# Optimization experiments

Measured on AMD Instinct MI355X. Metric: run time of the kernel, lower is better.

Reference implementation:

```python
import jax, jax.numpy as jnp
import numpy as np

REGION_INDEX = [[3,0,1,2,4],[7,8,9,10,11],[5,6],[13,12],[14,15,23,24,32,33],[22,21,31,30,40,39],[16,17,18,19,20],[25,26,27,28,29],[34,35,36,37,38],[41,42],[49,48],[43,44,45,46,47],[50,51,57],[56,55,61],[52,53,54],[58,59,60]]
INPUT_SIZE = 5
HIDDEN = 100
REGIONS = 16


def setup_inputs() -> dict:
    key = jax.random.key(0)
    ks = jax.random.split(key, 5)
    features = jax.random.normal(ks[0], (128, 256, 62, INPUT_SIZE), dtype=jnp.float32)
    s = 1.0 / np.sqrt(HIDDEN)  # PyTorch LSTM init scale
    # dir 0 = forward, dir 1 = reverse
    w_ih = jax.random.uniform(ks[1], (REGIONS, 2, 4 * HIDDEN, INPUT_SIZE), jnp.float32, -s, s)
    w_hh = jax.random.uniform(ks[2], (REGIONS, 2, 4 * HIDDEN, HIDDEN), jnp.float32, -s, s)
    b_ih = jax.random.uniform(ks[3], (REGIONS, 2, 4 * HIDDEN), jnp.float32, -s, s)
    b_hh = jax.random.uniform(ks[4], (REGIONS, 2, 4 * HIDDEN), jnp.float32, -s, s)
    return {"features": features, "w_ih": w_ih, "w_hh": w_hh, "b_ih": b_ih, "b_hh": b_hh}


def _lstm_last(x, Wih, Whh, bih, bhh):
    # x: (N, L, I) -> final hidden state h_{L-1}: (N, H). PyTorch gate order i,f,g,o.
    N = x.shape[0]
    H = Whh.shape[1]
    bias = bih + bhh

    def step(carry, xt):
        h, c = carry
        g = xt @ Wih.T + h @ Whh.T + bias
        i, f, gg, o = jnp.split(g, 4, axis=-1)
        c = jax.nn.sigmoid(f) * c + jax.nn.sigmoid(i) * jnp.tanh(gg)
        h = jax.nn.sigmoid(o) * jnp.tanh(c)
        return (h, c), None

    h0 = jnp.zeros((N, H), x.dtype)
    (h, _), _ = jax.lax.scan(step, (h0, h0), jnp.swapaxes(x, 0, 1))
    return h


def _forward(features, w_ih, w_hh, b_ih, b_hh):
    # flatten (B, T, 62, 5) -> (N, 62, 5)
    x = features.reshape(-1, features.shape[2], features.shape[3])
    outs = []
    for r in range(REGIONS):
        idx = jnp.asarray(REGION_INDEX[r])
        xr = x[:, idx, :]  # (N, L_r, 5)
        # forward-direction hidden at last timestep
        h_f = _lstm_last(xr, w_ih[r, 0], w_hh[r, 0], b_ih[r, 0], b_hh[r, 0])
        # reverse-direction output at last position == one step on x[:, -1] from zero state
        h_b = _lstm_last(xr[:, -1:, :], w_ih[r, 1], w_hh[r, 1], b_ih[r, 1], b_hh[r, 1])
        outs.append(jnp.concatenate([h_f, h_b], axis=-1))  # (N, 2H)
    return jnp.stack(outs, axis=1)  # (N, 16, 2H)


def reference(features, w_ih, w_hh, b_ih, b_hh):
    return _forward(features, w_ih, w_hh, b_ih, b_hh)
```

## Files before the change

### kernel.cpp

```cpp
#include <hip/hip_runtime.h>


typedef _Float16 f16;
typedef _Float16 half8 __attribute__((ext_vector_type(8)));
typedef float floatx4 __attribute__((ext_vector_type(4)));

#define FEAT_STRIDE 310
#define AST 136
#define ASZ (64 * AST)
#define OST 104

__constant__ int c_pos[16][6] = {
 {3,0,1,2,4,0},{7,8,9,10,11,0},{5,6,0,0,0,0},{13,12,0,0,0,0},
 {14,15,23,24,32,33},{22,21,31,30,40,39},{16,17,18,19,20,0},{25,26,27,28,29,0},
 {34,35,36,37,38,0},{41,42,0,0,0,0},{49,48,0,0,0,0},{43,44,45,46,47,0},
 {50,51,57,0,0,0},{56,55,61,0,0,0},{52,53,54,0,0,0},{58,59,60,0,0,0}};
__constant__ int c_len[16] = {5,5,2,2,6,6,5,5,5,2,2,5,3,3,3,3};

__device__ __forceinline__ float sigf(float x) {
  return __builtin_amdgcn_rcpf(1.f + __builtin_amdgcn_exp2f(-1.44269504088896f * x));
}
__device__ __forceinline__ float tanhf_fast(float x) {
  return 1.f - 2.f * __builtin_amdgcn_rcpf(1.f + __builtin_amdgcn_exp2f(2.88539008177793f * x));
}

__global__ __launch_bounds__(256) void prep_kernel(
    const float* __restrict__ w_ih, const float* __restrict__ w_hh,
    const float* __restrict__ b_ih, const float* __restrict__ b_hh,
    f16* __restrict__ wp)
{
  int id = blockIdx.x * 256 + threadIdx.x;
  if (id >= 16 * 400 * 128) return;
  int k = id & 127;
  int rowN = (id >> 7) % 400;
  int r = (id >> 7) / 400;
  int j = rowN >> 2, g = rowN & 3;
  int orig = (r * 2 + 0) * 400 + g * 100 + j;
  float v;
  if (k < 100)       v = w_hh[orig * 100 + k];
  else if (k < 105)  v = w_ih[orig * 5 + (k - 100)];
  else if (k == 105) v = b_ih[orig] + b_hh[orig];
  else               v = 0.f;
  wp[id] = (f16)v;
}

__global__ __launch_bounds__(320, 3) void fwd_kernel(
    const float* __restrict__ feat, const f16* __restrict__ wp,
    float* __restrict__ out)
{
  __shared__ __align__(16) f16 Abuf[2 * ASZ];
  float* smemf = (float*)Abuf;

  const int bx = blockIdx.x;
  const int r  = bx >> 9;
  const int n0 = (bx & 511) << 6;
  const int tid  = threadIdx.x;
  const int wave = tid >> 6;
  const int lane = tid & 63;
  const int quad = lane >> 4;
  const int l15  = lane & 15;
  const int T = c_len[r];

  half8 wf[5][4];
  {
    const f16* wr = wp + (size_t)r * 400 * 128;
    #pragma unroll
    for (int tn = 0; tn < 5; ++tn) {
      int row = 16 * (5 * wave + tn) + l15;
      #pragma unroll
      for (int kf = 0; kf < 4; ++kf)
        wf[tn][kf] = *(const half8*)(wr + row * 128 + 32 * kf + 8 * quad);
    }
  }

  for (int i = tid; i < 2 * 64 * 64; i += 320) {
    int buf = i >> 12;
    int rem = i & 4095;
    int m = rem >> 6, kw = rem & 63;
    ((unsigned int*)Abuf)[buf * (ASZ / 2) + m * (AST / 2) + kw] =
        (kw == 52) ? 0x3C000000u : 0u;
  }

  float xv[6];
  const int xm = tid & 63, xs = tid >> 6;
  {
    const float* fb = feat + (size_t)(n0 + xm) * FEAT_STRIDE + xs;
    #pragma unroll
    for (int tt = 0; tt < 6; ++tt)
      if (tt < T) xv[tt] = fb[c_pos[r][tt] * 5];
  }
  __syncthreads();
  Abuf[xm * AST + 100 + xs] = (f16)xv[0];
  __syncthreads();

  float creg[4][5];
  #pragma unroll
  for (int mt = 0; mt < 4; ++mt)
    #pragma unroll
    for (int tn = 0; tn < 5; ++tn) creg[mt][tn] = 0.f;

  for (int t = 0; t < T; ++t) {
    const f16* Acur = Abuf + (t & 1) * ASZ;
    f16* Anxt = Abuf + ((t + 1) & 1) * ASZ;

    if (t + 1 < T) {
      #pragma unroll
      for (int mt = 0; mt < 4; ++mt) {
        half8 bf[4];
        #pragma unroll
        for (int kf = 0; kf < 4; ++kf)
          bf[kf] = *(const half8*)(Acur + (16 * mt + l15) * AST + 32 * kf + 8 * quad);
        #pragma unroll
        for (int tn = 0; tn < 5; ++tn) {
          floatx4 acc = {0.f, 0.f, 0.f, 0.f};
          #pragma unroll
          for (int kf = 0; kf < 4; ++kf)
            acc = __builtin_amdgcn_mfma_f32_16x16x32_f16(wf[tn][kf], bf[kf], acc, 0, 0, 0);
          float ig = sigf(acc[0]);
          float fg = sigf(acc[1]);
          float gg = tanhf_fast(acc[2]);
          float og = sigf(acc[3]);
          float cn = fg * creg[mt][tn] + ig * gg;
          creg[mt][tn] = cn;
          int j = 4 * (5 * wave + tn) + quad;
          Anxt[(16 * mt + l15) * AST + j] = (f16)(og * tanhf_fast(cn));
        }
      }
      Anxt[xm * AST + 100 + xs] = (f16)xv[t + 1];
      __syncthreads();
    } else {
      float hreg[4][5];
      #pragma unroll
      for (int mt = 0; mt < 4; ++mt) {
        half8 bf[4];
        #pragma unroll
        for (int kf = 0; kf < 4; ++kf)
          bf[kf] = *(const half8*)(Acur + (16 * mt + l15) * AST + 32 * kf + 8 * quad);
        #pragma unroll
        for (int tn = 0; tn < 5; ++tn) {
          floatx4 acc = {0.f, 0.f, 0.f, 0.f};
          #pragma unroll
          for (int kf = 0; kf < 4; ++kf)
            acc = __builtin_amdgcn_mfma_f32_16x16x32_f16(wf[tn][kf], bf[kf], acc, 0, 0, 0);
          float ig = sigf(acc[0]);
          float fg = sigf(acc[1]);
          float gg = tanhf_fast(acc[2]);
          float og = sigf(acc[3]);
          float cn = fg * creg[mt][tn] + ig * gg;
          hreg[mt][tn] = og * tanhf_fast(cn);
        }
      }
      __syncthreads();
      #pragma unroll
      for (int mt = 0; mt < 4; ++mt)
        #pragma unroll
        for (int tn = 0; tn < 5; ++tn) {
          int j = 4 * (5 * wave + tn) + quad;
          smemf[(16 * mt + l15) * OST + j] = hreg[mt][tn];
        }
      __syncthreads();
    }
  }

  #pragma unroll
  for (int it = 0; it < 5; ++it) {
    int idx = tid + it * 320;
    int m = idx / 25, ch = idx - m * 25;
    floatx4 v = *(const floatx4*)(smemf + m * OST + ch * 4);
    *(floatx4*)(out + (size_t)(n0 + m) * 3200 + r * 200 + ch * 4) = v;
  }
}

__global__ __launch_bounds__(256) void bwd_kernel(
    const float* __restrict__ feat, const float* __restrict__ w_ih,
    const float* __restrict__ b_ih, const float* __restrict__ b_hh,
    float* __restrict__ out)
{
  __shared__ float wg[300 * 7];
  __shared__ float xs[128 * 5];
  const int bx = blockIdx.x;
  const int r  = bx >> 8;
  const int n0 = (bx & 255) << 7;
  const int tid = threadIdx.x;
  const int pos = c_pos[r][c_len[r] - 1];

  for (int i = tid; i < 2100; i += 256) {
    int row = i / 7, c = i - row * 7;
    int q = row / 100, jj = row - q * 100;
    int qq = (q == 0) ? 0 : (q + 1);
    int orig = (r * 2 + 1) * 400 + qq * 100 + jj;
    float v = 0.f;
    if (c < 5)       v = w_ih[orig * 5 + c];
    else if (c == 5) v = b_ih[orig] + b_hh[orig];
    wg[i] = v;
  }
  for (int i = tid; i < 640; i += 256) {
    int nl = i / 5, s = i - nl * 5;
    xs[i] = feat[(size_t)(n0 + nl) * FEAT_STRIDE + pos * 5 + s];
  }
  __syncthreads();

  if (tid < 200) {
    const int g  = tid / 100;
    const int jj = tid - g * 100;
    const float* wi = wg + jj * 7;
    const float* wc = wg + (100 + jj) * 7;
    const float* wo = wg + (200 + jj) * 7;
    float i0 = wi[0], i1 = wi[1], i2 = wi[2], i3 = wi[3], i4 = wi[4], ib = wi[5];
    float c0 = wc[0], c1 = wc[1], c2 = wc[2], c3 = wc[3], c4 = wc[4], cb = wc[5];
    float o0 = wo[0], o1 = wo[1], o2 = wo[2], o3 = wo[3], o4 = wo[4], ob = wo[5];
    for (int i = 0; i < 64; ++i) {
      int nl = g * 64 + i;
      const float* xp = xs + nl * 5;
      float x0 = xp[0], x1 = xp[1], x2 = xp[2], x3 = xp[3], x4 = xp[4];
      float gi = ib + i0*x0 + i1*x1 + i2*x2 + i3*x3 + i4*x4;
      float gc = cb + c0*x0 + c1*x1 + c2*x2 + c3*x3 + c4*x4;
      float go = ob + o0*x0 + o1*x1 + o2*x2 + o3*x3 + o4*x4;
      float cc = sigf(gi) * tanhf_fast(gc);
      float hh = sigf(go) * tanhf_fast(cc);
      out[(size_t)(n0 + nl) * 3200 + r * 200 + 100 + jj] = hh;
    }
  }
}

extern "C" void kernel_launch(void* const* d_in, const int* in_sizes, int n_in,
                              void* d_out, int out_size, void* d_ws, size_t ws_size,
                              hipStream_t stream) {
  const float* feat = (const float*)d_in[0];
  const float* w_ih = (const float*)d_in[1];
  const float* w_hh = (const float*)d_in[2];
  const float* b_ih = (const float*)d_in[3];
  const float* b_hh = (const float*)d_in[4];
  float* out = (float*)d_out;
  f16* wp = (f16*)d_ws;

  prep_kernel<<<3200, 256, 0, stream>>>(w_ih, w_hh, b_ih, b_hh, wp);
  fwd_kernel<<<8192, 320, 0, stream>>>(feat, wp, out);
  bwd_kernel<<<4096, 256, 0, stream>>>(feat, w_ih, b_ih, b_hh, out);
}
```

Measured before the change: 1.082 ms.

## Stage LSTM weights in LDS and run barrier-free per-wave recurrences

Each workgroup of 512 threads now copies the whole region weight matrix into LDS. Each wave then runs its own 16-row LSTM recurrence over all 400 gate rows in a private LDS state slice, with no block-wide barriers inside the time loop. The last hidden state is written straight to global memory instead of being staged through shared memory. The trade-off is that weight fragments are reloaded from LDS for every MFMA instead of staying in registers. The roughly 155 KB LDS footprint also limits occupancy to one block per CU.

```diff
diff --git a/kernel.cpp b/kernel.cpp
--- a/kernel.cpp
+++ b/kernel.cpp
@@ -6,9 +6,7 @@
 typedef float floatx4 __attribute__((ext_vector_type(4)));
 
 #define FEAT_STRIDE 310
-#define AST 136
-#define ASZ (64 * AST)
-#define OST 104
+#define WST 136
 
 __constant__ int c_pos[16][6] = {
  {3,0,1,2,4,0},{7,8,9,10,11,0},{5,6,0,0,0,0},{13,12,0,0,0,0},
@@ -44,16 +42,18 @@
   wp[id] = (f16)v;
 }
 
-__global__ __launch_bounds__(320, 3) void fwd_kernel(
+__global__ __launch_bounds__(512, 2) void fwd_kernel(
     const float* __restrict__ feat, const f16* __restrict__ wp,
     float* __restrict__ out)
 {
-  __shared__ __align__(16) f16 Abuf[2 * ASZ];
-  float* smemf = (float*)Abuf;
+  __shared__ __align__(16) unsigned char lds_raw[158976];
+  f16*   Wl = (f16*)lds_raw;
+  f16*   Sl = (f16*)(lds_raw + 108800);
+  float* Xl = (float*)(lds_raw + 143616);
 
   const int bx = blockIdx.x;
-  const int r  = bx >> 9;
-  const int n0 = (bx & 511) << 6;
+  const int r  = bx >> 8;
+  const int n0 = (bx & 255) << 7;
   const int tid  = threadIdx.x;
   const int wave = tid >> 6;
   const int lane = tid & 63;
@@ -61,113 +61,67 @@
   const int l15  = lane & 15;
   const int T = c_len[r];
 
-  half8 wf[5][4];
   {
     const f16* wr = wp + (size_t)r * 400 * 128;
-    #pragma unroll
-    for (int tn = 0; tn < 5; ++tn) {
-      int row = 16 * (5 * wave + tn) + l15;
-      #pragma unroll
-      for (int kf = 0; kf < 4; ++kf)
-        wf[tn][kf] = *(const half8*)(wr + row * 128 + 32 * kf + 8 * quad);
+    for (int idx = tid; idx < 400 * 16; idx += 512) {
+      int row = idx >> 4, c = idx & 15;
+      *(half8*)(Wl + row * WST + 8 * c) = *(const half8*)(wr + row * 128 + 8 * c);
     }
   }
-
-  for (int i = tid; i < 2 * 64 * 64; i += 320) {
-    int buf = i >> 12;
-    int rem = i & 4095;
-    int m = rem >> 6, kw = rem & 63;
-    ((unsigned int*)Abuf)[buf * (ASZ / 2) + m * (AST / 2) + kw] =
-        (kw == 52) ? 0x3C000000u : 0u;
+  for (int idx = tid; idx < T * 640; idx += 512) {
+    int t = idx / 640, rem = idx - t * 640;
+    int m = rem / 5, s = rem - m * 5;
+    Xl[idx] = feat[(size_t)(n0 + m) * FEAT_STRIDE + c_pos[r][t] * 5 + s];
   }
-
-  float xv[6];
-  const int xm = tid & 63, xs = tid >> 6;
   {
-    const float* fb = feat + (size_t)(n0 + xm) * FEAT_STRIDE + xs;
-    #pragma unroll
-    for (int tt = 0; tt < 6; ++tt)
-      if (tt < T) xv[tt] = fb[c_pos[r][tt] * 5];
+    unsigned int* Swd = (unsigned int*)Sl;
+    for (int idx = tid; idx < 8 * 16 * (WST / 2); idx += 512) {
+      int kw = idx % (WST / 2);
+      Swd[idx] = (kw == 52) ? 0x3C000000u : 0u;
+    }
   }
   __syncthreads();
-  Abuf[xm * AST + 100 + xs] = (f16)xv[0];
-  __syncthreads();
 
-  float creg[4][5];
+  f16* Sw = Sl + wave * 16 * WST;
+  const int xm = lane >> 2, xsl = lane & 3;
+
+  float creg[25];
   #pragma unroll
-  for (int mt = 0; mt < 4; ++mt)
-    #pragma unroll
-    for (int tn = 0; tn < 5; ++tn) creg[mt][tn] = 0.f;
+  for (int tn = 0; tn < 25; ++tn) creg[tn] = 0.f;
 
   for (int t = 0; t < T; ++t) {
-    const f16* Acur = Abuf + (t & 1) * ASZ;
-    f16* Anxt = Abuf + ((t + 1) & 1) * ASZ;
+    Sw[xm * WST + 100 + xsl] = (f16)Xl[t * 640 + (wave * 16 + xm) * 5 + xsl];
+    if (lane < 16)
+      Sw[l15 * WST + 104] = (f16)Xl[t * 640 + (wave * 16 + l15) * 5 + 4];
 
-    if (t + 1 < T) {
+    half8 bf[4];
+    #pragma unroll
+    for (int kf = 0; kf < 4; ++kf)
+      bf[kf] = *(const half8*)(Sw + l15 * WST + 32 * kf + 8 * quad);
+
+    const bool last = (t + 1 == T);
+    #pragma unroll
+    for (int tn = 0; tn < 25; ++tn) {
+      floatx4 acc = {0.f, 0.f, 0.f, 0.f};
       #pragma unroll
-      for (int mt = 0; mt < 4; ++mt) {
-        half8 bf[4];
-        #pragma unroll
-        for (int kf = 0; kf < 4; ++kf)
-          bf[kf] = *(const half8*)(Acur + (16 * mt + l15) * AST + 32 * kf + 8 * quad);
-        #pragma unroll
-        for (int tn = 0; tn < 5; ++tn) {
-          floatx4 acc = {0.f, 0.f, 0.f, 0.f};
-          #pragma unroll
-          for (int kf = 0; kf < 4; ++kf)
-            acc = __builtin_amdgcn_mfma_f32_16x16x32_f16(wf[tn][kf], bf[kf], acc, 0, 0, 0);
-          float ig = sigf(acc[0]);
-          float fg = sigf(acc[1]);
-          float gg = tanhf_fast(acc[2]);
-          float og = sigf(acc[3]);
-          float cn = fg * creg[mt][tn] + ig * gg;
-          creg[mt][tn] = cn;
-          int j = 4 * (5 * wave + tn) + quad;
-          Anxt[(16 * mt + l15) * AST + j] = (f16)(og * tanhf_fast(cn));
-        }
+      for (int kf = 0; kf < 4; ++kf) {
+        half8 wfr = *(const half8*)(Wl + (16 * tn + l15) * WST + 32 * kf + 8 * quad);
+        acc = __builtin_amdgcn_mfma_f32_16x16x32_f16(wfr, bf[kf], acc, 0, 0, 0);
       }
-      Anxt[xm * AST + 100 + xs] = (f16)xv[t + 1];
-      __syncthreads();
-    } else {
-      float hreg[4][5];
-      #pragma unroll
-      for (int mt = 0; mt < 4; ++mt) {
-        half8 bf[4];
-        #pragma unroll
-        for (int kf = 0; kf < 4; ++kf)
-          bf[kf] = *(const half8*)(Acur + (16 * mt + l15) * AST + 32 * kf + 8 * quad);
-        #pragma unroll
-        for (int tn = 0; tn < 5; ++tn) {
-          floatx4 acc = {0.f, 0.f, 0.f, 0.f};
-          #pragma unroll
-          for (int kf = 0; kf < 4; ++kf)
-            acc = __builtin_amdgcn_mfma_f32_16x16x32_f16(wf[tn][kf], bf[kf], acc, 0, 0, 0);
-          float ig = sigf(acc[0]);
-          float fg = sigf(acc[1]);
-          float gg = tanhf_fast(acc[2]);
-          float og = sigf(acc[3]);
-          float cn = fg * creg[mt][tn] + ig * gg;
-          hreg[mt][tn] = og * tanhf_fast(cn);
-        }
+      float ig = sigf(acc[0]);
+      float fg = sigf(acc[1]);
+      float gg = tanhf_fast(acc[2]);
+      float og = sigf(acc[3]);
+      float cn = fg * creg[tn] + ig * gg;
+      creg[tn] = cn;
+      float hv = og * tanhf_fast(cn);
+      int j = 4 * tn + quad;
+      if (!last) {
+        Sw[l15 * WST + j] = (f16)hv;
+      } else {
+        out[(size_t)(n0 + wave * 16 + l15) * 3200 + r * 200 + j] = hv;
       }
-      __syncthreads();
-      #pragma unroll
-      for (int mt = 0; mt < 4; ++mt)
-        #pragma unroll
-        for (int tn = 0; tn < 5; ++tn) {
-          int j = 4 * (5 * wave + tn) + quad;
-          smemf[(16 * mt + l15) * OST + j] = hreg[mt][tn];
-        }
-      __syncthreads();
     }
-  }
-
-  #pragma unroll
-  for (int it = 0; it < 5; ++it) {
-    int idx = tid + it * 320;
-    int m = idx / 25, ch = idx - m * 25;
-    floatx4 v = *(const floatx4*)(smemf + m * OST + ch * 4);
-    *(floatx4*)(out + (size_t)(n0 + m) * 3200 + r * 200 + ch * 4) = v;
   }
 }
 
@@ -235,6 +189,6 @@
   f16* wp = (f16*)d_ws;
 
   prep_kernel<<<3200, 256, 0, stream>>>(w_ih, w_hh, b_ih, b_hh, wp);
-  fwd_kernel<<<8192, 320, 0, stream>>>(feat, wp, out);
+  fwd_kernel<<<4096, 512, 0, stream>>>(feat, wp, out);
   bwd_kernel<<<4096, 256, 0, stream>>>(feat, w_ih, b_ih, b_hh, out);
 }
```

Measured after the change: 947.7 us. -12.4%, faster.
